# Performance work log

Measured on AMD Instinct MI355X. Metric: run time of the kernel, lower is better.

## Reference

```python
import jax, jax.numpy as jnp
import numpy as np

B, S, E, H = 2, 2048, 1024, 16
D = E // H  # head_dim = 64


def _rope_angles(seq_len, d, dtype=jnp.float32):
    # standard RoPE frequencies: theta_i = 10000^{-2i/d}
    inv_freq = 1.0 / (10000.0 ** (jnp.arange(0, d, 2, dtype=dtype) / d))  # [d/2]
    pos = jnp.arange(seq_len, dtype=dtype)                                # [S]
    ang = pos[:, None] * inv_freq[None, :]                                # [S, d/2]
    ang = jnp.concatenate([ang, ang], axis=-1)                            # [S, d]
    return jnp.cos(ang), jnp.sin(ang)


def _rotate_half(t):
    t1, t2 = jnp.split(t, 2, axis=-1)
    return jnp.concatenate([-t2, t1], axis=-1)


def _apply_rope(t, cos, sin):
    # t: [B, H, S, D]; cos/sin: [S, D]
    return t * cos[None, None, :, :] + _rotate_half(t) * sin[None, None, :, :]


def setup_inputs() -> dict:
    key = jax.random.key(0)
    ks = jax.random.split(key, 6)
    x = jax.random.normal(ks[0], (B, S, E), dtype=jnp.float32)
    mask = jnp.tril(jnp.ones((S, S), dtype=bool))  # causal: True = attend
    scale = 1.0 / np.sqrt(E)
    Wq = jax.random.normal(ks[1], (E, E), dtype=jnp.float32) * scale
    Wk = jax.random.normal(ks[2], (E, E), dtype=jnp.float32) * scale
    Wv = jax.random.normal(ks[3], (E, E), dtype=jnp.float32) * scale
    Wo = jax.random.normal(ks[4], (E, E), dtype=jnp.float32) * scale
    z = jnp.zeros((E,), dtype=jnp.float32)
    return {"x": x, "mask": mask, "Wq": Wq, "bq": z, "Wk": Wk, "bk": z,
            "Wv": Wv, "bv": z, "Wo": Wo, "bo": z}


def reference(x, mask, Wq, bq, Wk, bk, Wv, bv, Wo, bo):
    b, s, e = x.shape
    # QKV projections (nn.Linear convention: y = x @ W.T + b)
    def proj(W, bias):
        y = jnp.einsum('bse,fe->bsf', x, W) + bias
        return y.reshape(b, s, H, D).transpose(0, 2, 1, 3)  # [B,H,S,D]
    q, k, v = proj(Wq, bq), proj(Wk, bk), proj(Wv, bv)
    # RoPE on q and k (per-head rotary over head_dim)
    cos, sin = _rope_angles(s, D, dtype=x.dtype)
    q = _apply_rope(q, cos, sin)
    k = _apply_rope(k, cos, sin)
    # SDPA with boolean mask (True = attend)
    scores = jnp.einsum('bhqd,bhkd->bhqk', q, k) / jnp.sqrt(jnp.asarray(D, x.dtype))
    neg = jnp.asarray(jnp.finfo(x.dtype).min, x.dtype)
    scores = jnp.where(mask[None, None, :, :], scores, neg)
    attn = jax.nn.softmax(scores, axis=-1)
    out = jnp.einsum('bhqk,bhkd->bhqd', attn, v)          # [B,H,S,D]
    out = out.transpose(0, 2, 1, 3).reshape(b, s, e)       # [B,S,E]
    return jnp.einsum('bse,fe->bsf', out, Wo) + bo
```

## Files before the change

### kernel.cpp

```cpp
#include <hip/hip_runtime.h>
#include <hip/hip_bf16.h>

typedef unsigned short u16;
typedef unsigned int u32;
typedef __bf16 bf16x8 __attribute__((ext_vector_type(8)));
typedef float f32x4 __attribute__((ext_vector_type(4)));

#define S_LEN 2048
#define NHEAD 16
#define HDIM  64
#define EMB   1024
#define BATCH 2

__device__ __forceinline__ float bf2f(u16 u) {
  union { unsigned int i; float f; } c; c.i = ((unsigned int)u) << 16; return c.f;
}
__device__ __forceinline__ u16 f2bf(float f) {
  union { float f; unsigned int i; } c; c.f = f;
  unsigned int i = c.i;
  return (u16)((i + 0x7FFFu + ((i >> 16) & 1u)) >> 16);
}
__device__ __forceinline__ u16 f2bf_trunc(float f) {
  union { float f; unsigned int i; } c; c.f = f;
  return (u16)(c.i >> 16);
}
__device__ __forceinline__ f32x4 mfma16(bf16x8 a, bf16x8 b, f32x4 c) {
  return __builtin_amdgcn_mfma_f32_16x16x32_bf16(a, b, c, 0, 0, 0);
}
__device__ __forceinline__ void cp16(const u16* g, u16* l) {
  __builtin_amdgcn_global_load_lds(
      (const __attribute__((address_space(1))) u32*)g,
      (__attribute__((address_space(3))) u32*)l, 16, 0, 0);
}

__global__ __launch_bounds__(256) void convert_kernel(
    const void* __restrict__ x, const void* __restrict__ Wq,
    const void* __restrict__ Wk, const void* __restrict__ Wv,
    const void* __restrict__ Wo,
    u16* __restrict__ xb, u16* __restrict__ wqb, u16* __restrict__ wkb,
    u16* __restrict__ wvb, u16* __restrict__ wob,
    int* __restrict__ flag, float2* __restrict__ tab)
{
  __shared__ int s_flag;
  if (threadIdx.x == 0) s_flag = 0;
  __syncthreads();
  {
    const u16* xs = (const u16*)x;
    u16 w0 = xs[threadIdx.x * 2], w1 = xs[threadIdx.x * 2 + 1];
    if ((((w0 >> 7) & 0xFF) >= 0xC0) || (((w1 >> 7) & 0xFF) >= 0xC0))
      atomicOr(&s_flag, 1);
  }
  __syncthreads();
  const int f32io = s_flag;
  if (blockIdx.x == 0 && threadIdx.x == 0) flag[0] = f32io;

  size_t gid = (size_t)blockIdx.x * 256 + threadIdx.x;
  size_t e = gid * 8;
  const void* src; u16* dst; size_t off;
  if (e < 4194304) { src = x; dst = xb; off = e; }
  else {
    size_t rr = e - 4194304;
    int j = (int)(rr >> 20); off = rr & 1048575;
    src = (j == 0) ? Wq : (j == 1) ? Wk : (j == 2) ? Wv : Wo;
    dst = (j == 0) ? wqb : (j == 1) ? wkb : (j == 2) ? wvb : wob;
  }
  if (f32io) {
    const float* s = (const float*)src + off;
    float4 a = *(const float4*)s;
    float4 b2 = *(const float4*)(s + 4);
    ushort4 u0; u0.x = f2bf(a.x); u0.y = f2bf(a.y); u0.z = f2bf(a.z); u0.w = f2bf(a.w);
    ushort4 u1; u1.x = f2bf(b2.x); u1.y = f2bf(b2.y); u1.z = f2bf(b2.z); u1.w = f2bf(b2.w);
    *(ushort4*)(dst + off) = u0;
    *(ushort4*)(dst + off + 4) = u1;
  } else {
    *(uint4*)(dst + off) = *(const uint4*)((const u16*)src + off);
  }

  if (blockIdx.x < 256) {
    int id = blockIdx.x * 256 + threadIdx.x;
    int s = id >> 5, i = id & 31;
    float f = exp2f(-(float)i * 0.41524101186092029f);
    float ang = (float)s * f;
    tab[id] = make_float2(cosf(ang), sinf(ang));
  }
}

__device__ __forceinline__ void gemm_core_db(
    const u16* __restrict__ A, const u16* __restrict__ W,
    int m0, int n0, int t, f32x4 (&acc)[4][4],
    u16* __restrict__ Ash, u16* __restrict__ Bsh)
{
  const int lane = t & 63, lr = lane & 15, quad = lane >> 4;
  const int wv = t >> 6;
  const int wm = (wv & 1) * 64, wn = (wv >> 1) * 64;
  const int r0 = t >> 2, c0 = (t & 3) * 8;
  const int r1 = (t + 256) >> 2, c1 = (t & 3) * 8;
  const int lds0 = (t & 192) * 8;
  const int lds1 = (256 + (t & 192)) * 8;
  const u16* gA0 = A + (size_t)(m0 + r0) * 1024 + c0;
  const u16* gA1 = A + (size_t)(m0 + r1) * 1024 + c1;
  const u16* gB0 = W + (size_t)(n0 + r0) * 1024 + c0;
  const u16* gB1 = W + (size_t)(n0 + r1) * 1024 + c1;

  cp16(gA0, Ash + lds0); cp16(gA1, Ash + lds1);
  cp16(gB0, Bsh + lds0); cp16(gB1, Bsh + lds1);
  __syncthreads();

  for (int kt = 0; kt < 1024; kt += 32) {
    const int cur = (kt >> 5) & 1;
    const u16* Ac = Ash + cur * 4096;
    const u16* Bc = Bsh + cur * 4096;
    bf16x8 af[4], bfr[4];
#pragma unroll
    for (int mi = 0; mi < 4; ++mi)
      af[mi] = *(const bf16x8*)(Ac + (wm + mi * 16 + lr) * 32 + quad * 8);
#pragma unroll
    for (int ni = 0; ni < 4; ++ni)
      bfr[ni] = *(const bf16x8*)(Bc + (wn + ni * 16 + lr) * 32 + quad * 8);
    if (kt + 32 < 1024) {
      u16* An = Ash + (1 - cur) * 4096;
      u16* Bn = Bsh + (1 - cur) * 4096;
      cp16(gA0 + kt + 32, An + lds0); cp16(gA1 + kt + 32, An + lds1);
      cp16(gB0 + kt + 32, Bn + lds0); cp16(gB1 + kt + 32, Bn + lds1);
    }
#pragma unroll
    for (int mi = 0; mi < 4; ++mi)
#pragma unroll
      for (int ni = 0; ni < 4; ++ni)
        acc[mi][ni] = mfma16(af[mi], bfr[ni], acc[mi][ni]);
    __syncthreads();
  }
}

__device__ __forceinline__ void gemm_epilogue(
    int mode, int f32io, f32x4 (&acc)[4][4],
    const void* biasvp, void* outvp, int m0, int n0, int t,
    const float2* __restrict__ tab)
{
  const int lane = t & 63, lr = lane & 15, quad = lane >> 4;
  const int wv = t >> 6;
  const int wm = (wv & 1) * 64, wn = (wv >> 1) * 64;
  const float* biasf = (const float*)biasvp;
  const u16* biasb = (const u16*)biasvp;
#define BIASV(n) (f32io ? biasf[(n)] : bf2f(biasb[(n)]))
  if (mode == 1) {
    u16* Out = (u16*)outvp;
#pragma unroll
    for (int mi = 0; mi < 4; ++mi) {
#pragma unroll
      for (int r = 0; r < 4; ++r) {
        int mm = m0 + wm + mi * 16 + quad * 4 + r;
        int s = mm & (S_LEN - 1), b = mm >> 11;
        float2 cs0 = tab[s * 32 + lr];
        float2 cs1 = tab[s * 32 + 16 + lr];
#pragma unroll
        for (int ni = 0; ni < 4; ++ni) {
          int n = n0 + wn + ni * 16 + lr;
          int h = n >> 6, d = n & 63;
          float v  = acc[mi][ni][r]     + BIASV(n);
          float vp = acc[mi][ni ^ 2][r] + BIASV(n ^ 32);
          float rot = (d < 32) ? -vp : vp;
          float cc = (ni & 1) ? cs1.x : cs0.x;
          float ss = (ni & 1) ? cs1.y : cs0.y;
          size_t off = (((size_t)(b * NHEAD + h)) * S_LEN + s) * HDIM + d;
          Out[off] = f2bf(v * cc + rot * ss);
        }
      }
    }
  } else if (mode == 2) {
    u16* Out = (u16*)outvp;
#pragma unroll
    for (int mi = 0; mi < 4; ++mi) {
      int mm = m0 + wm + mi * 16 + quad * 4;
      int s = mm & (S_LEN - 1), b = mm >> 11;
#pragma unroll
      for (int ni = 0; ni < 4; ++ni) {
        int n = n0 + wn + ni * 16 + lr;
        int h = n >> 6, d = n & 63;
        float bv = BIASV(n);
        u16 p0 = f2bf(acc[mi][ni][0] + bv);
        u16 p1 = f2bf(acc[mi][ni][1] + bv);
        u16 p2 = f2bf(acc[mi][ni][2] + bv);
        u16 p3 = f2bf(acc[mi][ni][3] + bv);
        uint2 pk = make_uint2((u32)p0 | ((u32)p1 << 16),
                              (u32)p2 | ((u32)p3 << 16));
        size_t off = (((size_t)(b * NHEAD + h)) * HDIM + d) * S_LEN + s;
        *(uint2*)(Out + off) = pk;
      }
    }
  }
#undef BIASV
}

__global__ __launch_bounds__(256) void gemm_qkv(
    const u16* __restrict__ A, const u16* __restrict__ Wq,
    const u16* __restrict__ Wk, const u16* __restrict__ Wv,
    const void* bq, const void* bk, const void* bv,
    u16* qo, u16* ko, u16* vo, const int* __restrict__ dflag,
    const float2* __restrict__ tab)
{
  alignas(16) __shared__ u16 Ash[2 * 128 * 32];
  alignas(16) __shared__ u16 Bsh[2 * 128 * 32];
  const int wsel = blockIdx.x >> 3;
  const u16* W = (wsel == 0) ? Wq : (wsel == 1) ? Wk : Wv;
  const void* bias = (wsel == 0) ? bq : (wsel == 1) ? bk : bv;
  void* out = (wsel == 0) ? (void*)qo : (wsel == 1) ? (void*)ko : (void*)vo;
  const int mode = (wsel == 2) ? 2 : 1;
  const int m0 = blockIdx.y * 128, n0 = (blockIdx.x & 7) * 128;
  f32x4 acc[4][4];
  const f32x4 zero4 = {0.f, 0.f, 0.f, 0.f};
#pragma unroll
  for (int i = 0; i < 4; ++i)
#pragma unroll
    for (int j = 0; j < 4; ++j) acc[i][j] = zero4;
  gemm_core_db(A, W, m0, n0, threadIdx.x, acc, Ash, Bsh);
  gemm_epilogue(mode, dflag[0], acc, bias, out, m0, n0, threadIdx.x, tab);
}

__global__ __launch_bounds__(256) void gemm_out(
    const u16* __restrict__ A, const u16* __restrict__ W,
    const void* bias, void* out, const int* __restrict__ dflag)
{
  alignas(16) __shared__ u16 Ash[2 * 64 * 32];
  alignas(16) __shared__ u16 Bsh[2 * 128 * 32];
  const int t = threadIdx.x, lane = t & 63, wv = t >> 6;
  const int lr = lane & 15, quad = lane >> 4;
  const int m0 = blockIdx.y * 64, n0 = blockIdx.x * 128;
  const int wm = (wv & 1) * 32, wn = (wv >> 1) * 64;
  const int f32io = dflag[0];

  const int r0 = t >> 2, c0 = (t & 3) * 8;
  const int r1 = (t + 256) >> 2;
  const int lds0 = (t & 192) * 8;
  const int lds1 = (256 + (t & 192)) * 8;
  const u16* gA0 = A + (size_t)(m0 + (r0 & 63)) * 1024 + c0;
  const u16* gB0 = W + (size_t)(n0 + r0) * 1024 + c0;
  const u16* gB1 = W + (size_t)(n0 + r1) * 1024 + c0;

  f32x4 acc[2][4];
  const f32x4 zero4 = {0.f, 0.f, 0.f, 0.f};
#pragma unroll
  for (int i = 0; i < 2; ++i)
#pragma unroll
    for (int j = 0; j < 4; ++j) acc[i][j] = zero4;

  cp16(gA0, Ash + lds0);
  cp16(gB0, Bsh + lds0); cp16(gB1, Bsh + lds1);
  __syncthreads();

  for (int kt = 0; kt < 1024; kt += 32) {
    const int cur = (kt >> 5) & 1;
    const u16* Ac = Ash + cur * 2048;
    const u16* Bc = Bsh + cur * 4096;
    bf16x8 af[2], bfr[4];
#pragma unroll
    for (int mi = 0; mi < 2; ++mi)
      af[mi] = *(const bf16x8*)(Ac + (wm + mi * 16 + lr) * 32 + quad * 8);
#pragma unroll
    for (int ni = 0; ni < 4; ++ni)
      bfr[ni] = *(const bf16x8*)(Bc + (wn + ni * 16 + lr) * 32 + quad * 8);
    if (kt + 32 < 1024) {
      u16* An = Ash + (1 - cur) * 2048;
      u16* Bn = Bsh + (1 - cur) * 4096;
      cp16(gA0 + kt + 32, An + lds0);
      cp16(gB0 + kt + 32, Bn + lds0); cp16(gB1 + kt + 32, Bn + lds1);
    }
#pragma unroll
    for (int mi = 0; mi < 2; ++mi)
#pragma unroll
      for (int ni = 0; ni < 4; ++ni)
        acc[mi][ni] = mfma16(af[mi], bfr[ni], acc[mi][ni]);
    __syncthreads();
  }

  const float* biasf = (const float*)bias;
  const u16* biasb = (const u16*)bias;
  float* Outf = (float*)out;
  u16* Outb = (u16*)out;
#pragma unroll
  for (int mi = 0; mi < 2; ++mi) {
#pragma unroll
    for (int r = 0; r < 4; ++r) {
      int mm = m0 + wm + mi * 16 + quad * 4 + r;
#pragma unroll
      for (int ni = 0; ni < 4; ++ni) {
        int n = n0 + wn + ni * 16 + lr;
        float bv = f32io ? biasf[n] : bf2f(biasb[n]);
        float v = acc[mi][ni][r] + bv;
        size_t off = (size_t)mm * 1024 + n;
        if (f32io) Outf[off] = v; else Outb[off] = f2bf(v);
      }
    }
  }
}

__device__ __forceinline__ void attn_phase(
    const bf16x8 (&qf)[2], f32x4 (&oacc)[4], float& lsum,
    const u16 (*__restrict__ Ksh)[72], const u16 (*__restrict__ Vsh)[72],
    u16 (*__restrict__ Pw)[72],
    int kv0, int q0w, bool diag, int lr, int quad)
{
  const f32x4 zero4 = {0.f, 0.f, 0.f, 0.f};
  f32x4 sc[4];
#pragma unroll
  for (int ni = 0; ni < 4; ++ni) {
    bf16x8 kf0 = *(const bf16x8*)&Ksh[ni * 16 + lr][quad * 8];
    bf16x8 kf1 = *(const bf16x8*)&Ksh[ni * 16 + lr][32 + quad * 8];
    f32x4 z = zero4;
    z = mfma16(kf0, qf[0], z);
    z = mfma16(kf1, qf[1], z);
    sc[ni] = z;
  }
  const int qa = q0w + lr;
  if (diag) {
#pragma unroll
    for (int ni = 0; ni < 4; ++ni)
#pragma unroll
      for (int r = 0; r < 4; ++r) {
        float sarg = sc[ni][r] * 0.18033688f - 21.64042561f;
        if (kv0 + ni * 16 + quad * 4 + r > qa) sarg = -1e4f;
        float p = exp2f(sarg);
        sc[ni][r] = p;
        lsum += p;
      }
  } else {
#pragma unroll
    for (int ni = 0; ni < 4; ++ni)
#pragma unroll
      for (int r = 0; r < 4; ++r) {
        float p = exp2f(sc[ni][r] * 0.18033688f - 21.64042561f);
        sc[ni][r] = p;
        lsum += p;
      }
  }
#pragma unroll
  for (int ni = 0; ni < 4; ++ni) {
    u32 lo = (u32)f2bf_trunc(sc[ni][0]) | ((u32)f2bf_trunc(sc[ni][1]) << 16);
    u32 hi = (u32)f2bf_trunc(sc[ni][2]) | ((u32)f2bf_trunc(sc[ni][3]) << 16);
    *(uint2*)&Pw[lr][ni * 16 + quad * 4] = make_uint2(lo, hi);
  }
  bf16x8 pa0 = *(const bf16x8*)&Pw[lr][quad * 8];
  bf16x8 pa1 = *(const bf16x8*)&Pw[lr][32 + quad * 8];
#pragma unroll
  for (int oni = 0; oni < 4; ++oni) {
    bf16x8 vf0 = *(const bf16x8*)&Vsh[oni * 16 + lr][quad * 8];
    bf16x8 vf1 = *(const bf16x8*)&Vsh[oni * 16 + lr][32 + quad * 8];
    oacc[oni] = mfma16(pa0, vf0, oacc[oni]);
    oacc[oni] = mfma16(pa1, vf1, oacc[oni]);
  }
}

__device__ __forceinline__ void attn_phase_half(
    const bf16x8 (&qf)[2], f32x4 (&oacc)[4], float& lsum,
    const u16 (*__restrict__ Ksh)[72], const u16 (*__restrict__ Vsh)[72],
    u16 (*__restrict__ Pw)[72],
    int kv0, int q0w, bool diag, int half, int lr, int quad)
{
  const f32x4 zero4 = {0.f, 0.f, 0.f, 0.f};
  f32x4 sc[2];
#pragma unroll
  for (int i = 0; i < 2; ++i) {
    const int ni = half * 2 + i;
    bf16x8 kf0 = *(const bf16x8*)&Ksh[ni * 16 + lr][quad * 8];
    bf16x8 kf1 = *(const bf16x8*)&Ksh[ni * 16 + lr][32 + quad * 8];
    f32x4 z = zero4;
    z = mfma16(kf0, qf[0], z);
    z = mfma16(kf1, qf[1], z);
    sc[i] = z;
  }
  const int qa = q0w + lr;
  if (diag) {
#pragma unroll
    for (int i = 0; i < 2; ++i)
#pragma unroll
      for (int r = 0; r < 4; ++r) {
        float sarg = sc[i][r] * 0.18033688f - 21.64042561f;
        if (kv0 + (half * 2 + i) * 16 + quad * 4 + r > qa) sarg = -1e4f;
        float p = exp2f(sarg);
        sc[i][r] = p;
        lsum += p;
      }
  } else {
#pragma unroll
    for (int i = 0; i < 2; ++i)
#pragma unroll
      for (int r = 0; r < 4; ++r) {
        float p = exp2f(sc[i][r] * 0.18033688f - 21.64042561f);
        sc[i][r] = p;
        lsum += p;
      }
  }
#pragma unroll
  for (int i = 0; i < 2; ++i) {
    u32 lo = (u32)f2bf_trunc(sc[i][0]) | ((u32)f2bf_trunc(sc[i][1]) << 16);
    u32 hi = (u32)f2bf_trunc(sc[i][2]) | ((u32)f2bf_trunc(sc[i][3]) << 16);
    *(uint2*)&Pw[lr][(half * 2 + i) * 16 + quad * 4] = make_uint2(lo, hi);
  }
  bf16x8 pa = *(const bf16x8*)&Pw[lr][half * 32 + quad * 8];
#pragma unroll
  for (int oni = 0; oni < 4; ++oni) {
    bf16x8 vf = *(const bf16x8*)&Vsh[oni * 16 + lr][half * 32 + quad * 8];
    oacc[oni] = mfma16(pa, vf, oacc[oni]);
  }
}

__device__ __forceinline__ void attn_finish(
    f32x4 (&oacc)[4], float lsum, u16* __restrict__ O,
    int bh, int q0w, int lr, int quad)
{
  const int b = bh >> 4, h = bh & 15;
  lsum += __shfl_xor(lsum, 16);
  lsum += __shfl_xor(lsum, 32);
  const float inv = 1.f / lsum;
#pragma unroll
  for (int r = 0; r < 4; ++r) {
    const float scale = __shfl(inv, quad * 4 + r);
#pragma unroll
    for (int oni = 0; oni < 4; ++oni) {
      int s = q0w + quad * 4 + r;
      int e = h * HDIM + oni * 16 + lr;
      O[((size_t)(b * S_LEN + s)) * EMB + e] = f2bf(oacc[oni][r] * scale);
    }
  }
}

__global__ __launch_bounds__(512, 4) void attn_kernel(
    const u16* __restrict__ Q, const u16* __restrict__ Kr,
    const u16* __restrict__ Vt, u16* __restrict__ O)
{
  alignas(16) __shared__ u16 Kdb[2][64][72];
  alignas(16) __shared__ u16 Vdb[2][64][72];
  alignas(16) __shared__ u16 Psh[8][16][72];
  const int t = threadIdx.x, lane = t & 63, wv = t >> 6;
  const int lr = lane & 15, quad = lane >> 4;
  const int bh = blockIdx.y;
  const int qtA = blockIdx.x;
  const int qtB = 31 - qtA;
  const bool grpA = (wv < 4);
  const int q0own = (grpA ? qtA : qtB) * 64 + (wv & 3) * 16;
  const int q0B = qtB * 64 + (wv & 3) * 16;
  const size_t base = (size_t)bh * S_LEN * HDIM;

  bf16x8 qfO[2], qfH[2];
  {
    const u16* qrow = Q + base + (size_t)(q0own + lr) * HDIM + quad * 8;
    qfO[0] = *(const bf16x8*)qrow;
    qfO[1] = *(const bf16x8*)(qrow + 32);
  }
  if (grpA) {
    const u16* qrow = Q + base + (size_t)(q0B + lr) * HDIM + quad * 8;
    qfH[0] = *(const bf16x8*)qrow;
    qfH[1] = *(const bf16x8*)(qrow + 32);
  } else { qfH[0] = qfO[0]; qfH[1] = qfO[1]; }

  f32x4 oacc0[4], oacc1[4];
  float lsum0 = 0.f, lsum1 = 0.f;
  const f32x4 zero4 = {0.f, 0.f, 0.f, 0.f};
#pragma unroll
  for (int i = 0; i < 4; ++i) { oacc0[i] = zero4; oacc1[i] = zero4; }

  const int rr = t >> 3, cc = (t & 7) * 8;
  uint4 krg = *(const uint4*)(Kr + base + (size_t)rr * HDIM + cc);
  uint4 vrg = *(const uint4*)(Vt + base + (size_t)rr * S_LEN + cc);

  for (int j = 0; j <= qtB; ++j) {
    const int cur = j & 1;
    *(uint4*)&Kdb[cur][rr][cc] = krg;
    *(uint4*)&Vdb[cur][rr][cc] = vrg;
    __syncthreads();
    if (j < qtB) {
      const int kv1 = (j + 1) * 64;
      krg = *(const uint4*)(Kr + base + (size_t)(kv1 + rr) * HDIM + cc);
      vrg = *(const uint4*)(Vt + base + (size_t)rr * S_LEN + kv1 + cc);
    }
    if (j <= qtA) {
      attn_phase(qfO, oacc0, lsum0, Kdb[cur], Vdb[cur], Psh[wv],
                 j * 64, q0own, grpA && (j == qtA), lr, quad);
    } else if (grpA) {
      attn_phase_half(qfH, oacc1, lsum1, Kdb[cur], Vdb[cur], Psh[wv],
                      j * 64, q0B, j == qtB, 1, lr, quad);
    } else {
      attn_phase_half(qfO, oacc0, lsum0, Kdb[cur], Vdb[cur], Psh[wv],
                      j * 64, q0B, j == qtB, 0, lr, quad);
    }
  }

  __syncthreads();
  if (grpA) {
    float* dst = (float*)&Psh[0][0][0] + (size_t)(wv * 64 + lane) * 17;
#pragma unroll
    for (int oni = 0; oni < 4; ++oni)
#pragma unroll
      for (int r = 0; r < 4; ++r) dst[oni * 4 + r] = oacc1[oni][r];
    dst[16] = lsum1;
  }
  __syncthreads();
  if (!grpA) {
    const float* src =
        (const float*)&Psh[0][0][0] + (size_t)((wv - 4) * 64 + lane) * 17;
#pragma unroll
    for (int oni = 0; oni < 4; ++oni)
#pragma unroll
      for (int r = 0; r < 4; ++r) oacc0[oni][r] += src[oni * 4 + r];
    lsum0 += src[16];
  }
  attn_finish(oacc0, lsum0, O, bh, q0own, lr, quad);
}

extern "C" void kernel_launch(void* const* d_in, const int* in_sizes, int n_in,
                              void* d_out, int out_size, void* d_ws, size_t ws_size,
                              hipStream_t stream) {
  const void* x  = d_in[0];
  const void* Wq = d_in[2]; const void* bq = d_in[3];
  const void* Wk = d_in[4]; const void* bk = d_in[5];
  const void* Wv = d_in[6]; const void* bv = d_in[7];
  const void* Wo = d_in[8]; const void* bo = d_in[9];

  char* ws = (char*)d_ws;
  int* flag = (int*)ws;
  u16* xb  = (u16*)(ws + 256);
  u16* qws = xb  + 4194304;
  u16* kws = qws + 4194304;
  u16* vws = kws + 4194304;
  u16* wqb = vws + 4194304;
  u16* wkb = wqb + 1048576;
  u16* wvb = wkb + 1048576;
  u16* wob = wvb + 1048576;
  float2* tab = (float2*)(wob + 1048576);
  u16* ows = xb;

  convert_kernel<<<4096, 256, 0, stream>>>(x, Wq, Wk, Wv, Wo,
                                           xb, wqb, wkb, wvb, wob, flag, tab);
  gemm_qkv<<<dim3(24, 32), 256, 0, stream>>>(xb, wqb, wkb, wvb,
                                             bq, bk, bv, qws, kws, vws, flag, tab);
  attn_kernel<<<dim3(16, 32), 512, 0, stream>>>(qws, kws, vws, ows);
  gemm_out<<<dim3(8, 64), 256, 0, stream>>>(ows, wob, bo, d_out, flag);
}
```

Before: 208.5 us.

## Triple-buffer GEMM K-loop with explicit vmcnt waits and reuse it for output projection

Replaces the double-buffered GEMM main loop with a three-stage LDS ring. It prefetches two K-tiles ahead and uses explicit s_waitcnt vmcnt plus raw s_barrier instead of __syncthreads, and raises wave priority around the MFMA block. The output projection GEMM now reuses this core with 128x128 tiles and a new generic epilogue mode, so it launches half as many blocks. This aims to hide global load latency better, at the cost of more LDS per block, which may reduce occupancy, and fewer blocks for the output GEMM.

```diff
diff --git a/kernel.cpp b/kernel.cpp
--- a/kernel.cpp
+++ b/kernel.cpp
@@ -32,6 +32,12 @@
       (const __attribute__((address_space(1))) u32*)g,
       (__attribute__((address_space(3))) u32*)l, 16, 0, 0);
 }
+#define WAITV(N) do { \
+  asm volatile("s_waitcnt vmcnt(" #N ")" ::: "memory"); \
+  __builtin_amdgcn_sched_barrier(0); } while (0)
+#define BARRIER() do { \
+  __builtin_amdgcn_s_barrier(); \
+  __builtin_amdgcn_sched_barrier(0); } while (0)
 
 __global__ __launch_bounds__(256) void convert_kernel(
     const void* __restrict__ x, const void* __restrict__ Wq,
@@ -85,7 +91,7 @@
   }
 }
 
-__device__ __forceinline__ void gemm_core_db(
+__device__ __forceinline__ void gemm_core_p3(
     const u16* __restrict__ A, const u16* __restrict__ W,
     int m0, int n0, int t, f32x4 (&acc)[4][4],
     u16* __restrict__ Ash, u16* __restrict__ Bsh)
@@ -94,20 +100,23 @@
   const int wv = t >> 6;
   const int wm = (wv & 1) * 64, wn = (wv >> 1) * 64;
   const int r0 = t >> 2, c0 = (t & 3) * 8;
-  const int r1 = (t + 256) >> 2, c1 = (t & 3) * 8;
+  const int r1 = (t + 256) >> 2;
   const int lds0 = (t & 192) * 8;
   const int lds1 = (256 + (t & 192)) * 8;
   const u16* gA0 = A + (size_t)(m0 + r0) * 1024 + c0;
-  const u16* gA1 = A + (size_t)(m0 + r1) * 1024 + c1;
+  const u16* gA1 = A + (size_t)(m0 + r1) * 1024 + c0;
   const u16* gB0 = W + (size_t)(n0 + r0) * 1024 + c0;
-  const u16* gB1 = W + (size_t)(n0 + r1) * 1024 + c1;
+  const u16* gB1 = W + (size_t)(n0 + r1) * 1024 + c0;
 
   cp16(gA0, Ash + lds0); cp16(gA1, Ash + lds1);
   cp16(gB0, Bsh + lds0); cp16(gB1, Bsh + lds1);
-  __syncthreads();
-
+  cp16(gA0 + 32, Ash + 4096 + lds0); cp16(gA1 + 32, Ash + 4096 + lds1);
+  cp16(gB0 + 32, Bsh + 4096 + lds0); cp16(gB1 + 32, Bsh + 4096 + lds1);
+  WAITV(4);
+  BARRIER();
+
+  int cur = 0;
   for (int kt = 0; kt < 1024; kt += 32) {
-    const int cur = (kt >> 5) & 1;
     const u16* Ac = Ash + cur * 4096;
     const u16* Bc = Bsh + cur * 4096;
     bf16x8 af[4], bfr[4];
@@ -117,18 +126,25 @@
 #pragma unroll
     for (int ni = 0; ni < 4; ++ni)
       bfr[ni] = *(const bf16x8*)(Bc + (wn + ni * 16 + lr) * 32 + quad * 8);
-    if (kt + 32 < 1024) {
-      u16* An = Ash + (1 - cur) * 4096;
-      u16* Bn = Bsh + (1 - cur) * 4096;
-      cp16(gA0 + kt + 32, An + lds0); cp16(gA1 + kt + 32, An + lds1);
-      cp16(gB0 + kt + 32, Bn + lds0); cp16(gB1 + kt + 32, Bn + lds1);
-    }
+    if (kt + 64 < 1024) {
+      int nx = cur + 2; if (nx >= 3) nx -= 3;
+      u16* An = Ash + nx * 4096;
+      u16* Bn = Bsh + nx * 4096;
+      cp16(gA0 + kt + 64, An + lds0); cp16(gA1 + kt + 64, An + lds1);
+      cp16(gB0 + kt + 64, Bn + lds0); cp16(gB1 + kt + 64, Bn + lds1);
+    }
+    __builtin_amdgcn_s_setprio(1);
 #pragma unroll
     for (int mi = 0; mi < 4; ++mi)
 #pragma unroll
       for (int ni = 0; ni < 4; ++ni)
         acc[mi][ni] = mfma16(af[mi], bfr[ni], acc[mi][ni]);
-    __syncthreads();
+    __builtin_amdgcn_s_setprio(0);
+    if (kt + 32 < 1024) {
+      if (kt + 64 < 1024) { WAITV(4); } else { WAITV(0); }
+      BARRIER();
+    }
+    cur = (cur + 1 >= 3) ? 0 : cur + 1;
   }
 }
 
@@ -188,6 +204,23 @@
         *(uint2*)(Out + off) = pk;
       }
     }
+  } else {
+    float* Outf = (float*)outvp;
+    u16* Outb = (u16*)outvp;
+#pragma unroll
+    for (int mi = 0; mi < 4; ++mi) {
+#pragma unroll
+      for (int r = 0; r < 4; ++r) {
+        int mm = m0 + wm + mi * 16 + quad * 4 + r;
+#pragma unroll
+        for (int ni = 0; ni < 4; ++ni) {
+          int n = n0 + wn + ni * 16 + lr;
+          float v = acc[mi][ni][r] + BIASV(n);
+          size_t off = (size_t)mm * 1024 + n;
+          if (f32io) Outf[off] = v; else Outb[off] = f2bf(v);
+        }
+      }
+    }
   }
 #undef BIASV
 }
@@ -199,8 +232,8 @@
     u16* qo, u16* ko, u16* vo, const int* __restrict__ dflag,
     const float2* __restrict__ tab)
 {
-  alignas(16) __shared__ u16 Ash[2 * 128 * 32];
-  alignas(16) __shared__ u16 Bsh[2 * 128 * 32];
+  alignas(16) __shared__ u16 Ash[3 * 128 * 32];
+  alignas(16) __shared__ u16 Bsh[3 * 128 * 32];
   const int wsel = blockIdx.x >> 3;
   const u16* W = (wsel == 0) ? Wq : (wsel == 1) ? Wk : Wv;
   const void* bias = (wsel == 0) ? bq : (wsel == 1) ? bk : bv;
@@ -213,7 +246,7 @@
   for (int i = 0; i < 4; ++i)
 #pragma unroll
     for (int j = 0; j < 4; ++j) acc[i][j] = zero4;
-  gemm_core_db(A, W, m0, n0, threadIdx.x, acc, Ash, Bsh);
+  gemm_core_p3(A, W, m0, n0, threadIdx.x, acc, Ash, Bsh);
   gemm_epilogue(mode, dflag[0], acc, bias, out, m0, n0, threadIdx.x, tab);
 }
 
@@ -221,77 +254,17 @@
     const u16* __restrict__ A, const u16* __restrict__ W,
     const void* bias, void* out, const int* __restrict__ dflag)
 {
-  alignas(16) __shared__ u16 Ash[2 * 64 * 32];
-  alignas(16) __shared__ u16 Bsh[2 * 128 * 32];
-  const int t = threadIdx.x, lane = t & 63, wv = t >> 6;
-  const int lr = lane & 15, quad = lane >> 4;
-  const int m0 = blockIdx.y * 64, n0 = blockIdx.x * 128;
-  const int wm = (wv & 1) * 32, wn = (wv >> 1) * 64;
-  const int f32io = dflag[0];
-
-  const int r0 = t >> 2, c0 = (t & 3) * 8;
-  const int r1 = (t + 256) >> 2;
-  const int lds0 = (t & 192) * 8;
-  const int lds1 = (256 + (t & 192)) * 8;
-  const u16* gA0 = A + (size_t)(m0 + (r0 & 63)) * 1024 + c0;
-  const u16* gB0 = W + (size_t)(n0 + r0) * 1024 + c0;
-  const u16* gB1 = W + (size_t)(n0 + r1) * 1024 + c0;
-
-  f32x4 acc[2][4];
+  alignas(16) __shared__ u16 Ash[3 * 128 * 32];
+  alignas(16) __shared__ u16 Bsh[3 * 128 * 32];
+  const int m0 = blockIdx.y * 128, n0 = blockIdx.x * 128;
+  f32x4 acc[4][4];
   const f32x4 zero4 = {0.f, 0.f, 0.f, 0.f};
 #pragma unroll
-  for (int i = 0; i < 2; ++i)
+  for (int i = 0; i < 4; ++i)
 #pragma unroll
     for (int j = 0; j < 4; ++j) acc[i][j] = zero4;
-
-  cp16(gA0, Ash + lds0);
-  cp16(gB0, Bsh + lds0); cp16(gB1, Bsh + lds1);
-  __syncthreads();
-
-  for (int kt = 0; kt < 1024; kt += 32) {
-    const int cur = (kt >> 5) & 1;
-    const u16* Ac = Ash + cur * 2048;
-    const u16* Bc = Bsh + cur * 4096;
-    bf16x8 af[2], bfr[4];
-#pragma unroll
-    for (int mi = 0; mi < 2; ++mi)
-      af[mi] = *(const bf16x8*)(Ac + (wm + mi * 16 + lr) * 32 + quad * 8);
-#pragma unroll
-    for (int ni = 0; ni < 4; ++ni)
-      bfr[ni] = *(const bf16x8*)(Bc + (wn + ni * 16 + lr) * 32 + quad * 8);
-    if (kt + 32 < 1024) {
-      u16* An = Ash + (1 - cur) * 2048;
-      u16* Bn = Bsh + (1 - cur) * 4096;
-      cp16(gA0 + kt + 32, An + lds0);
-      cp16(gB0 + kt + 32, Bn + lds0); cp16(gB1 + kt + 32, Bn + lds1);
-    }
-#pragma unroll
-    for (int mi = 0; mi < 2; ++mi)
-#pragma unroll
-      for (int ni = 0; ni < 4; ++ni)
-        acc[mi][ni] = mfma16(af[mi], bfr[ni], acc[mi][ni]);
-    __syncthreads();
-  }
-
-  const float* biasf = (const float*)bias;
-  const u16* biasb = (const u16*)bias;
-  float* Outf = (float*)out;
-  u16* Outb = (u16*)out;
-#pragma unroll
-  for (int mi = 0; mi < 2; ++mi) {
-#pragma unroll
-    for (int r = 0; r < 4; ++r) {
-      int mm = m0 + wm + mi * 16 + quad * 4 + r;
-#pragma unroll
-      for (int ni = 0; ni < 4; ++ni) {
-        int n = n0 + wn + ni * 16 + lr;
-        float bv = f32io ? biasf[n] : bf2f(biasb[n]);
-        float v = acc[mi][ni][r] + bv;
-        size_t off = (size_t)mm * 1024 + n;
-        if (f32io) Outf[off] = v; else Outb[off] = f2bf(v);
-      }
-    }
-  }
+  gemm_core_p3(A, W, m0, n0, threadIdx.x, acc, Ash, Bsh);
+  gemm_epilogue(0, dflag[0], acc, bias, out, m0, n0, threadIdx.x, nullptr);
 }
 
 __device__ __forceinline__ void attn_phase(
@@ -534,5 +507,5 @@
   gemm_qkv<<<dim3(24, 32), 256, 0, stream>>>(xb, wqb, wkb, wvb,
                                              bq, bk, bv, qws, kws, vws, flag, tab);
   attn_kernel<<<dim3(16, 32), 512, 0, stream>>>(qws, kws, vws, ows);
-  gemm_out<<<dim3(8, 64), 256, 0, stream>>>(ows, wob, bo, d_out, flag);
-}
+  gemm_out<<<dim3(8, 32), 256, 0, stream>>>(ows, wob, bo, d_out, flag);
+}
```

Result: slower. 245.0 us (+17.5%).

## Swizzle GEMM LDS tiles and remap block indices for XCD-local L2 reuse

Applied to the files above, without the earlier changes.

The GEMM kernels now XOR-swizzle the 16-byte chunk column within each LDS row, both when staging global data and when reading MFMA fragments. This is meant to cut LDS bank conflicts on the fragment reads. All three kernels (QKV GEMM, output GEMM, attention) also remap the linear block id so that blocks landing on the same XCD share M tiles or heads, aiming for better L2 locality on the multi-die MI355X. The remapping assumes round-robin block-to-XCD dispatch and fixed grid shapes, and if either assumption fails it would miss tiles or compute the wrong ones.

```diff
diff --git a/kernel.cpp b/kernel.cpp
--- a/kernel.cpp
+++ b/kernel.cpp
@@ -93,14 +93,16 @@
   const int lane = t & 63, lr = lane & 15, quad = lane >> 4;
   const int wv = t >> 6;
   const int wm = (wv & 1) * 64, wn = (wv >> 1) * 64;
-  const int r0 = t >> 2, c0 = (t & 3) * 8;
-  const int r1 = (t + 256) >> 2, c1 = (t & 3) * 8;
+  const int r0 = t >> 2;
+  const int r1 = (t + 256) >> 2;
+  const int c0 = (((t & 3) ^ ((t >> 2) & 3))) * 8;
   const int lds0 = (t & 192) * 8;
   const int lds1 = (256 + (t & 192)) * 8;
+  const int qx = ((quad ^ (lr & 3))) * 8;
   const u16* gA0 = A + (size_t)(m0 + r0) * 1024 + c0;
-  const u16* gA1 = A + (size_t)(m0 + r1) * 1024 + c1;
+  const u16* gA1 = A + (size_t)(m0 + r1) * 1024 + c0;
   const u16* gB0 = W + (size_t)(n0 + r0) * 1024 + c0;
-  const u16* gB1 = W + (size_t)(n0 + r1) * 1024 + c1;
+  const u16* gB1 = W + (size_t)(n0 + r1) * 1024 + c0;
 
   cp16(gA0, Ash + lds0); cp16(gA1, Ash + lds1);
   cp16(gB0, Bsh + lds0); cp16(gB1, Bsh + lds1);
@@ -113,10 +115,10 @@
     bf16x8 af[4], bfr[4];
 #pragma unroll
     for (int mi = 0; mi < 4; ++mi)
-      af[mi] = *(const bf16x8*)(Ac + (wm + mi * 16 + lr) * 32 + quad * 8);
+      af[mi] = *(const bf16x8*)(Ac + (wm + mi * 16 + lr) * 32 + qx);
 #pragma unroll
     for (int ni = 0; ni < 4; ++ni)
-      bfr[ni] = *(const bf16x8*)(Bc + (wn + ni * 16 + lr) * 32 + quad * 8);
+      bfr[ni] = *(const bf16x8*)(Bc + (wn + ni * 16 + lr) * 32 + qx);
     if (kt + 32 < 1024) {
       u16* An = Ash + (1 - cur) * 4096;
       u16* Bn = Bsh + (1 - cur) * 4096;
@@ -201,12 +203,16 @@
 {
   alignas(16) __shared__ u16 Ash[2 * 128 * 32];
   alignas(16) __shared__ u16 Bsh[2 * 128 * 32];
-  const int wsel = blockIdx.x >> 3;
+  const int lin = blockIdx.y * 24 + blockIdx.x;
+  const int xcd = lin & 7, rr = lin >> 3;
+  const int mt = (xcd << 2) + (rr & 3);
+  const int nw = rr >> 2;
+  const int wsel = nw >> 3;
   const u16* W = (wsel == 0) ? Wq : (wsel == 1) ? Wk : Wv;
   const void* bias = (wsel == 0) ? bq : (wsel == 1) ? bk : bv;
   void* out = (wsel == 0) ? (void*)qo : (wsel == 1) ? (void*)ko : (void*)vo;
   const int mode = (wsel == 2) ? 2 : 1;
-  const int m0 = blockIdx.y * 128, n0 = (blockIdx.x & 7) * 128;
+  const int m0 = mt * 128, n0 = (nw & 7) * 128;
   f32x4 acc[4][4];
   const f32x4 zero4 = {0.f, 0.f, 0.f, 0.f};
 #pragma unroll
@@ -225,14 +231,19 @@
   alignas(16) __shared__ u16 Bsh[2 * 128 * 32];
   const int t = threadIdx.x, lane = t & 63, wv = t >> 6;
   const int lr = lane & 15, quad = lane >> 4;
-  const int m0 = blockIdx.y * 64, n0 = blockIdx.x * 128;
+  const int lin = blockIdx.y * 8 + blockIdx.x;
+  const int xcd = lin & 7, rl = lin >> 3;
+  const int mt = (xcd << 3) + (rl & 7);
+  const int m0 = mt * 64, n0 = (rl >> 3) * 128;
   const int wm = (wv & 1) * 32, wn = (wv >> 1) * 64;
   const int f32io = dflag[0];
 
-  const int r0 = t >> 2, c0 = (t & 3) * 8;
+  const int r0 = t >> 2;
   const int r1 = (t + 256) >> 2;
+  const int c0 = (((t & 3) ^ ((t >> 2) & 3))) * 8;
   const int lds0 = (t & 192) * 8;
   const int lds1 = (256 + (t & 192)) * 8;
+  const int qx = ((quad ^ (lr & 3))) * 8;
   const u16* gA0 = A + (size_t)(m0 + (r0 & 63)) * 1024 + c0;
   const u16* gB0 = W + (size_t)(n0 + r0) * 1024 + c0;
   const u16* gB1 = W + (size_t)(n0 + r1) * 1024 + c0;
@@ -255,10 +266,10 @@
     bf16x8 af[2], bfr[4];
 #pragma unroll
     for (int mi = 0; mi < 2; ++mi)
-      af[mi] = *(const bf16x8*)(Ac + (wm + mi * 16 + lr) * 32 + quad * 8);
+      af[mi] = *(const bf16x8*)(Ac + (wm + mi * 16 + lr) * 32 + qx);
 #pragma unroll
     for (int ni = 0; ni < 4; ++ni)
-      bfr[ni] = *(const bf16x8*)(Bc + (wn + ni * 16 + lr) * 32 + quad * 8);
+      bfr[ni] = *(const bf16x8*)(Bc + (wn + ni * 16 + lr) * 32 + qx);
     if (kt + 32 < 1024) {
       u16* An = Ash + (1 - cur) * 2048;
       u16* Bn = Bsh + (1 - cur) * 4096;
@@ -433,8 +444,10 @@
   alignas(16) __shared__ u16 Psh[8][16][72];
   const int t = threadIdx.x, lane = t & 63, wv = t >> 6;
   const int lr = lane & 15, quad = lane >> 4;
-  const int bh = blockIdx.y;
-  const int qtA = blockIdx.x;
+  const int lin = blockIdx.y * 16 + blockIdx.x;
+  const int xcd = lin & 7, rl = lin >> 3;
+  const int bh = (xcd << 2) + (rl & 3);
+  const int qtA = rl >> 2;
   const int qtB = 31 - qtA;
   const bool grpA = (wv < 4);
   const int q0own = (grpA ? qtA : qtB) * 64 + (wv & 3) * 16;
```

Result: faster. 202.4 us (-2.9%).
